# Optimization experiments

Hardware: AMD Instinct MI355X
Metric: run time of the kernel (lower is better)

Reference implementation:

```python
import jax, jax.numpy as jnp
import numpy as np

N_NODES = 100000
N_EDGES = 3200000
N_GRAPHS = 512


def setup_inputs() -> dict:
    key = jax.random.key(0)
    k1, k2, k3, k4, k5 = jax.random.split(key, 5)
    x = jax.random.normal(k1, (N_NODES, 5), dtype=jnp.float32)
    edge_index = jax.random.randint(k2, (2, N_EDGES), 0, N_NODES, dtype=jnp.int64)
    batch = jnp.sort(jax.random.randint(k3, (N_NODES,), 0, N_GRAPHS, dtype=jnp.int64))
    W1 = jax.random.normal(k4, (5, 16), dtype=jnp.float32) * (1.0 / np.sqrt(5.0))
    b1 = jnp.zeros((16,), dtype=jnp.float32)
    W2 = jax.random.normal(k5, (16, 16), dtype=jnp.float32) * 0.25
    b2 = jnp.zeros((16,), dtype=jnp.float32)
    return {"x": x, "edge_index": edge_index, "batch": batch,
            "W1": W1, "b1": b1, "W2": W2, "b2": b2}


def _gcn_conv(x, src, dst, norm, W, b, n_nodes):
    # PyG GCNConv: h = X W; out_i = sum_{j->i} norm_ij * h_j + b
    h = x @ W                                   # [N, out]
    msgs = h[src] * norm[:, None]               # gather + scale  [E_tot, out]
    out = jax.ops.segment_sum(msgs, dst, num_segments=n_nodes)
    return out + b


def reference(x, edge_index, batch, W1, b1, W2, b2):
    n = x.shape[0]
    # add self-loops (GCNConv default)
    loops = jnp.arange(n, dtype=edge_index.dtype)
    src = jnp.concatenate([edge_index[0], loops])
    dst = jnp.concatenate([edge_index[1], loops])
    # symmetric normalization: deg computed on destination nodes
    deg = jax.ops.segment_sum(jnp.ones_like(src, dtype=x.dtype), dst, num_segments=n)
    dinv = jnp.where(deg > 0, jax.lax.rsqrt(deg), 0.0)
    norm = dinv[src] * dinv[dst]                # [E_tot]

    h = jax.nn.relu(_gcn_conv(x, src, dst, norm, W1, b1, n))
    h = jax.nn.relu(_gcn_conv(h, src, dst, norm, W2, b2, n))

    # global mean pool over graphs in the batch
    sums = jax.ops.segment_sum(h, batch, num_segments=N_GRAPHS)
    cnts = jax.ops.segment_sum(jnp.ones((n,), dtype=h.dtype), batch, num_segments=N_GRAPHS)
    return sums / jnp.maximum(cnts, 1.0)[:, None]
```

## Files before the change

kernel.cpp:

```cpp
#include <hip/hip_runtime.h>

#define N_NODES  100000
#define N_EDGES  3200000
#define N_GRAPHS 512
#define F_IN     5
#define F_HID    16

#define PBLK   512
#define CHUNK  8192
#define NCHUNK ((N_EDGES + CHUNK - 1) / CHUNK)
#define BKT_NODES 256
#define NBKT ((N_NODES + BKT_NODES - 1) / BKT_NODES)
#define SHARDS 8
#define CAP_S  1280
#define CAP    (SHARDS * CAP_S)


__device__ inline unsigned short f2bf(float f) {
    unsigned u = __float_as_uint(f);
    return (unsigned short)((u + 0x7fffu + ((u >> 16) & 1u)) >> 16);
}
__device__ inline float bf2f(unsigned short h) {
    return __uint_as_float(((unsigned)h) << 16);
}
__device__ inline float4 cvt4(ushort4 u) {
    return make_float4(bf2f(u.x), bf2f(u.y), bf2f(u.z), bf2f(u.w));
}
__device__ inline float4 shfl_xor4(float4 v, int m) {
    return make_float4(__shfl_xor(v.x, m, 64), __shfl_xor(v.y, m, 64),
                       __shfl_xor(v.z, m, 64), __shfl_xor(v.w, m, 64));
}

template <int NW>
__device__ inline int block_incl_scan(int v, int t, int* wsum) {
    int lane = t & 63, wave = t >> 6;
    int x = v;
#pragma unroll
    for (int o = 1; o < 64; o <<= 1) {
        int y = __shfl_up(x, o, 64);
        if (lane >= o) x += y;
    }
    if (lane == 63) wsum[wave] = x;
    __syncthreads();
    if (t < 64) {
        int w = (t < NW) ? wsum[t] : 0;
#pragma unroll
        for (int o = 1; o < NW; o <<= 1) {
            int y = __shfl_up(w, o, 64);
            if (t >= o) w += y;
        }
        if (t < NW) wsum[t] = w;
    }
    __syncthreads();
    return x + (wave ? wsum[wave - 1] : 0);
}

__device__ inline float4 row_gather8s(const ushort4* __restrict__ pb4, int i, int j,
                                      int half, int beg, int len,
                                      const int* __restrict__ col) {
    float4 acc = half ? make_float4(0.f, 0.f, 0.f, 0.f)
                      : cvt4(pb4[i * 4 + j]);
    for (int k = half * 8; k < len; k += 16) {
        int4 c0 = *(const int4*)(col + beg + k);
        int4 c1 = *(const int4*)(col + beg + k + 4);
        ushort4 a0 = pb4[c0.x * 4 + j], a1 = pb4[c0.y * 4 + j];
        ushort4 a2 = pb4[c0.z * 4 + j], a3 = pb4[c0.w * 4 + j];
        ushort4 a4 = pb4[c1.x * 4 + j], a5 = pb4[c1.y * 4 + j];
        ushort4 a6 = pb4[c1.z * 4 + j], a7 = pb4[c1.w * 4 + j];
        float4 f0 = cvt4(a0), f1 = cvt4(a1), f2 = cvt4(a2), f3 = cvt4(a3);
        float4 f4 = cvt4(a4), f5 = cvt4(a5), f6 = cvt4(a6), f7 = cvt4(a7);
        acc.x += ((f0.x + f1.x) + (f2.x + f3.x)) + ((f4.x + f5.x) + (f6.x + f7.x));
        acc.y += ((f0.y + f1.y) + (f2.y + f3.y)) + ((f4.y + f5.y) + (f6.y + f7.y));
        acc.z += ((f0.z + f1.z) + (f2.z + f3.z)) + ((f4.z + f5.z) + (f6.z + f7.z));
        acc.w += ((f0.w + f1.w) + (f2.w + f3.w)) + ((f4.w + f5.w) + (f6.w + f7.w));
    }
    return acc;
}


__global__ void k_zero(int* __restrict__ cursor, float* __restrict__ out,
                       float* __restrict__ cnt, unsigned short* __restrict__ pb_a,
                       unsigned short* __restrict__ pb_b) {
    int i = blockIdx.x * blockDim.x + threadIdx.x;
    if (i < NBKT * SHARDS) cursor[i] = 0;
    if (i < N_GRAPHS * F_HID) out[i] = 0.0f;
    if (i < N_GRAPHS) cnt[i] = 0.0f;
    if (i < F_HID) {
        pb_a[(size_t)N_NODES * F_HID + i] = 0;
        pb_b[(size_t)N_NODES * F_HID + i] = 0;
    }
}

__global__ __launch_bounds__(PBLK) void k_part(const int* __restrict__ src,
                                               const int* __restrict__ dst,
                                               const int* __restrict__ batch,
                                               int* __restrict__ cursor,
                                               unsigned* __restrict__ packed,
                                               float* __restrict__ cnt) {
    __shared__ int hist[PBLK];
    __shared__ int scn[PBLK];
    __shared__ int rnk[PBLK];
    __shared__ int gbase[PBLK];
    __shared__ int wsum[8];
    __shared__ int bcnt[8];
    __shared__ int g0s;
    int t = threadIdx.x;
    int blk = blockIdx.x;
    int s = blk & (SHARDS - 1);
    int chunk0 = blk * CHUNK;
    int n = min(CHUNK, N_EDGES - chunk0);
    hist[t] = 0;
    if (t < 8) bcnt[t] = 0;
    if (t == 0) {
        int nb = blk * BKT_NODES;
        g0s = batch[nb < N_NODES ? nb : N_NODES - 1];
    }
    __syncthreads();
    int ls[CHUNK / PBLK], ld[CHUNK / PBLK];
    for (int k = t, idx = 0; k < n; k += PBLK, idx++) {
        ls[idx] = src[chunk0 + k];
        ld[idx] = dst[chunk0 + k];
        atomicAdd(&hist[ld[idx] >> 8], 1);
    }
    if (t < BKT_NODES) {
        int i2 = blk * BKT_NODES + t;
        if (i2 < N_NODES) {
            int g = batch[i2];
            int l = g - g0s;
            if (l >= 0 && l < 8) atomicAdd(&bcnt[l], 1);
            else atomicAdd(&cnt[g], 1.0f);
        }
    }
    __syncthreads();
    int v = hist[t];
    int incl = block_incl_scan<8>(v, t, wsum);
    int excl = incl - v;
    scn[t] = excl;
    rnk[t] = excl;
    gbase[t] = (v > 0) ? atomicAdd(&cursor[t * SHARDS + s], v) : 0;
    if (t < 8 && bcnt[t] > 0) atomicAdd(&cnt[g0s + t], (float)bcnt[t]);
    __syncthreads();
    for (int k = t, idx = 0; k < n; k += PBLK, idx++) {
        int d = ld[idx], sr = ls[idx];
        int b = d >> 8;
        int r = atomicAdd(&rnk[b], 1);
        int g = gbase[b] + (r - scn[b]);
        if (g < CAP_S)
            packed[(size_t)b * CAP + s * CAP_S + g] =
                ((unsigned)sr << 8) | (unsigned)(d & 255);
    }
}

__global__ __launch_bounds__(512) void k_csr(const int* __restrict__ cursor,
                                             const unsigned* __restrict__ packed,
                                             const float* __restrict__ x,
                                             const float* __restrict__ W1,
                                             int2* __restrict__ rowbc,
                                             int* __restrict__ col,
                                             float* __restrict__ dinv,
                                             unsigned short* __restrict__ pb) {
    __shared__ int hist[BKT_NODES];
    __shared__ int rnk[BKT_NODES];
    __shared__ int wsum[8];
    __shared__ int ns[SHARDS];
    __shared__ float w1[F_IN * F_HID];
    int b = blockIdx.x, t = threadIdx.x;
    int base = b * CAP;
    if (t < BKT_NODES) hist[t] = 0;
    if (t < SHARDS) ns[t] = min(cursor[b * SHARDS + t], CAP_S);
    if (t >= 512 - F_IN * F_HID) w1[t - (512 - F_IN * F_HID)] = W1[t - (512 - F_IN * F_HID)];
    __syncthreads();
    const unsigned* pk = packed + (size_t)b * CAP;
#pragma unroll
    for (int s = 0; s < SHARDS; s++) {
        int m = ns[s];
        const unsigned* pks = pk + s * CAP_S;
        for (int k = t; k < m; k += 512)
            atomicAdd(&hist[pks[k] & 255], 1);
    }
    __syncthreads();
    int v = (t < BKT_NODES) ? hist[t] : 0;
    int len = (v + 7) & ~7;
    int incl = block_incl_scan<8>(len, t, wsum);
    int excl = incl - len;
    if (t < BKT_NODES) rnk[t] = excl;
    __syncthreads();
#pragma unroll
    for (int s = 0; s < SHARDS; s++) {
        int m = ns[s];
        const unsigned* pks = pk + s * CAP_S;
        for (int k = t; k < m; k += 512) {
            unsigned w = pks[k];
            int r = atomicAdd(&rnk[w & 255], 1);
            if (r < CAP) col[base + r] = (int)(w >> 8);
        }
    }
    if (t < BKT_NODES) {
        int node = b * BKT_NODES + t;
        if (node < N_NODES) {
            int mylen = min(len, ((CAP - min(excl, CAP)) & ~7));
            for (int q = v; q < mylen; q++) {
                int r = excl + q;
                if (r < CAP) col[base + r] = N_NODES;
            }
            rowbc[node] = make_int2(base + excl, mylen);
            float di = rsqrtf((float)(1 + v));
            dinv[node] = di;
            float xi[F_IN];
#pragma unroll
            for (int k = 0; k < F_IN; k++) xi[k] = x[node * F_IN + k];
            float hv[F_HID];
#pragma unroll
            for (int c = 0; c < F_HID; c++) {
                float h = 0.0f;
#pragma unroll
                for (int k = 0; k < F_IN; k++) h += xi[k] * w1[k * F_HID + c];
                hv[c] = h * di;
            }
            unsigned pkk[8];
#pragma unroll
            for (int q = 0; q < 8; q++)
                pkk[q] = (unsigned)f2bf(hv[2 * q]) | ((unsigned)f2bf(hv[2 * q + 1]) << 16);
            uint4* d4 = (uint4*)(pb + (size_t)node * F_HID);
            d4[0] = make_uint4(pkk[0], pkk[1], pkk[2], pkk[3]);
            d4[1] = make_uint4(pkk[4], pkk[5], pkk[6], pkk[7]);
        }
    }
}

__global__ __launch_bounds__(256) void k_pull_mid(const int2* __restrict__ rowbc,
                                                  const int* __restrict__ col,
                                                  const unsigned short* __restrict__ pb,
                                                  const float* __restrict__ dinv,
                                                  const float* __restrict__ W2,
                                                  const float* __restrict__ b1,
                                                  unsigned short* __restrict__ pb2) {
    __shared__ float w[F_HID * F_HID];
    __shared__ float bb[F_HID];
    int t = threadIdx.x;
    w[t] = W2[t];
    if (t < F_HID) bb[t] = b1[t];
    __syncthreads();
    int gid = blockIdx.x * 256 + t;
    int i = gid >> 3;
    int half = (gid >> 2) & 1;
    int j = gid & 3;
    int2 rc = rowbc[i];
    float4 acc = row_gather8s((const ushort4*)pb, i, j, half, rc.x, rc.y, col);
    acc.x += __shfl_xor(acc.x, 4, 64);
    acc.y += __shfl_xor(acc.y, 4, 64);
    acc.z += __shfl_xor(acc.z, 4, 64);
    acc.w += __shfl_xor(acc.w, 4, 64);
    float di = dinv[i];
    float4 mine;
    mine.x = fmaxf(di * acc.x + bb[4 * j + 0], 0.0f);
    mine.y = fmaxf(di * acc.y + bb[4 * j + 1], 0.0f);
    mine.z = fmaxf(di * acc.z + bb[4 * j + 2], 0.0f);
    mine.w = fmaxf(di * acc.w + bb[4 * j + 3], 0.0f);
    float4 o1 = shfl_xor4(mine, 1);
    float4 o2 = shfl_xor4(mine, 2);
    float4 o3 = shfl_xor4(mine, 3);
    float4 hq0 = (j == 0) ? mine : ((j == 1) ? o1 : ((j == 2) ? o2 : o3));
    float4 hq1 = (j == 1) ? mine : ((j == 0) ? o1 : ((j == 3) ? o2 : o3));
    float4 hq2 = (j == 2) ? mine : ((j == 3) ? o1 : ((j == 0) ? o2 : o3));
    float4 hq3 = (j == 3) ? mine : ((j == 2) ? o1 : ((j == 1) ? o2 : o3));
    float hc[F_HID] = {hq0.x, hq0.y, hq0.z, hq0.w, hq1.x, hq1.y, hq1.z, hq1.w,
                       hq2.x, hq2.y, hq2.z, hq2.w, hq3.x, hq3.y, hq3.z, hq3.w};
    float m0 = 0.0f, m1 = 0.0f, m2 = 0.0f, m3 = 0.0f;
#pragma unroll
    for (int c = 0; c < F_HID; c++) {
        float4 wv = *(const float4*)&w[c * F_HID + 4 * j];
        float hv = hc[c];
        m0 += hv * wv.x; m1 += hv * wv.y; m2 += hv * wv.z; m3 += hv * wv.w;
    }
    if (half == 0) {
        unsigned p0 = (unsigned)f2bf(m0 * di) | ((unsigned)f2bf(m1 * di) << 16);
        unsigned p1 = (unsigned)f2bf(m2 * di) | ((unsigned)f2bf(m3 * di) << 16);
        *(uint2*)(pb2 + (size_t)i * F_HID + 4 * j) = make_uint2(p0, p1);
    }
}

__global__ __launch_bounds__(256) void k_pull_pool(const int2* __restrict__ rowbc,
                                                   const int* __restrict__ col,
                                                   const unsigned short* __restrict__ pb,
                                                   const float* __restrict__ dinv,
                                                   const int* __restrict__ batch,
                                                   const float* __restrict__ b2,
                                                   const float* __restrict__ cnt,
                                                   float* __restrict__ out) {
    __shared__ float bb[F_HID];
    __shared__ float acc2[8][F_HID];
    __shared__ int gcnt[8];
    __shared__ int g0s;
    int t = threadIdx.x;
    if (t < F_HID) bb[t] = b2[t];
    if (t < 8) gcnt[t] = 0;
    if (t < 8 * F_HID) ((float*)acc2)[t] = 0.0f;
    int blk0node = blockIdx.x * 32;
    if (t == 0) g0s = batch[blk0node < N_NODES ? blk0node : N_NODES - 1];
    __syncthreads();
    int g0 = g0s;
    int gid = blockIdx.x * 256 + t;
    int i = gid >> 3;
    int half = (gid >> 2) & 1;
    int j = gid & 3;
    int2 rc = rowbc[i];
    float4 acc = row_gather8s((const ushort4*)pb, i, j, half, rc.x, rc.y, col);
    acc.x += __shfl_xor(acc.x, 4, 64);
    acc.y += __shfl_xor(acc.y, 4, 64);
    acc.z += __shfl_xor(acc.z, 4, 64);
    acc.w += __shfl_xor(acc.w, 4, 64);
    if (half == 0) {
        float di = dinv[i];
        float h0 = fmaxf(di * acc.x + bb[4 * j + 0], 0.0f);
        float h1 = fmaxf(di * acc.y + bb[4 * j + 1], 0.0f);
        float h2 = fmaxf(di * acc.z + bb[4 * j + 2], 0.0f);
        float h3 = fmaxf(di * acc.w + bb[4 * j + 3], 0.0f);
        int g = batch[i];
        int l = g - g0;
        if (l >= 0 && l < 8) {
            atomicAdd(&acc2[l][4 * j + 0], h0);
            atomicAdd(&acc2[l][4 * j + 1], h1);
            atomicAdd(&acc2[l][4 * j + 2], h2);
            atomicAdd(&acc2[l][4 * j + 3], h3);
            if (j == 0) atomicAdd(&gcnt[l], 1);
        } else {
            float inv = 1.0f / cnt[g];
            atomicAdd(&out[g * F_HID + 4 * j + 0], h0 * inv);
            atomicAdd(&out[g * F_HID + 4 * j + 1], h1 * inv);
            atomicAdd(&out[g * F_HID + 4 * j + 2], h2 * inv);
            atomicAdd(&out[g * F_HID + 4 * j + 3], h3 * inv);
        }
    }
    __syncthreads();
    if (t < 8 * F_HID) {
        int l = t >> 4, c = t & 15;
        if (gcnt[l] > 0) {
            float inv = 1.0f / cnt[g0 + l];
            atomicAdd(&out[(g0 + l) * F_HID + c], acc2[l][c] * inv);
        }
    }
}


extern "C" void kernel_launch(void* const* d_in, const int* in_sizes, int n_in,
                              void* d_out, int out_size, void* d_ws, size_t ws_size,
                              hipStream_t stream) {
    const float* x     = (const float*)d_in[0];
    const int*   ei    = (const int*)d_in[1];
    const int*   batch = (const int*)d_in[2];
    const float* W1    = (const float*)d_in[3];
    const float* b1    = (const float*)d_in[4];
    const float* W2    = (const float*)d_in[5];
    const float* b2    = (const float*)d_in[6];
    float* out = (float*)d_out;

    int*            cursor = (int*)d_ws;
    unsigned*       packed = (unsigned*)(cursor + 3200);
    int2*           rowbc  = (int2*)(packed + (size_t)NBKT * CAP);
    int*            col    = (int*)(rowbc + N_NODES);
    float*          dinv   = (float*)(col + (size_t)NBKT * CAP);
    unsigned short* pb_a   = (unsigned short*)(dinv + N_NODES);
    unsigned short* pb_b   = pb_a + (size_t)(N_NODES + 1) * F_HID;
    float*          cnt    = (float*)(pb_b + (size_t)(N_NODES + 1) * F_HID);

    const int* src = ei;
    const int* dst = ei + N_EDGES;

    const int nb_pull = (N_NODES * 8) / 256;

    k_zero<<<(N_GRAPHS * F_HID + 255) / 256, 256, 0, stream>>>(cursor, out, cnt,
                                                               pb_a, pb_b);
    k_part<<<NCHUNK, PBLK, 0, stream>>>(src, dst, batch, cursor, packed, cnt);
    k_csr<<<NBKT, 512, 0, stream>>>(cursor, packed, x, W1, rowbc, col, dinv, pb_a);
    k_pull_mid<<<nb_pull, 256, 0, stream>>>(rowbc, col, pb_a, dinv, W2, b1, pb_b);
    k_pull_pool<<<nb_pull, 256, 0, stream>>>(rowbc, col, pb_b, dinv, batch, b2,
                                             cnt, out);
}
```

Before: 189.8 us.

## Reuse histogram atomic ranks in partition and CSR kernels to skip second atomic pass

Each edge now keeps the return value of its first shared-memory histogram atomicAdd as its local rank. This removes the block scan and the second atomic rank pass in k_part, and the reread of packed data in k_csr. k_part's chunk size is halved so more blocks run, and the per-block graph-count range shrinks to 128 nodes to match. k_csr holds its packed words in registers across the scan, which costs more registers and may lower occupancy.

```diff
diff --git a/kernel.cpp b/kernel.cpp
--- a/kernel.cpp
+++ b/kernel.cpp
@@ -7,13 +7,16 @@
 #define F_HID    16
 
 #define PBLK   512
-#define CHUNK  8192
+#define CHUNK  4096
+#define EPT    (CHUNK / PBLK)
 #define NCHUNK ((N_EDGES + CHUNK - 1) / CHUNK)
+#define CNT_NODES 128
 #define BKT_NODES 256
 #define NBKT ((N_NODES + BKT_NODES - 1) / BKT_NODES)
 #define SHARDS 8
 #define CAP_S  1280
 #define CAP    (SHARDS * CAP_S)
+#define UNR    (CAP / 512)
 
 
 __device__ inline unsigned short f2bf(float f) {
@@ -98,10 +101,7 @@
                                                unsigned* __restrict__ packed,
                                                float* __restrict__ cnt) {
     __shared__ int hist[PBLK];
-    __shared__ int scn[PBLK];
-    __shared__ int rnk[PBLK];
     __shared__ int gbase[PBLK];
-    __shared__ int wsum[8];
     __shared__ int bcnt[8];
     __shared__ int g0s;
     int t = threadIdx.x;
@@ -112,18 +112,22 @@
     hist[t] = 0;
     if (t < 8) bcnt[t] = 0;
     if (t == 0) {
-        int nb = blk * BKT_NODES;
+        int nb = blk * CNT_NODES;
         g0s = batch[nb < N_NODES ? nb : N_NODES - 1];
     }
     __syncthreads();
-    int ls[CHUNK / PBLK], ld[CHUNK / PBLK];
-    for (int k = t, idx = 0; k < n; k += PBLK, idx++) {
-        ls[idx] = src[chunk0 + k];
-        ld[idx] = dst[chunk0 + k];
-        atomicAdd(&hist[ld[idx] >> 8], 1);
-    }
-    if (t < BKT_NODES) {
-        int i2 = blk * BKT_NODES + t;
+    int ls[EPT], ld[EPT], lr[EPT];
+#pragma unroll
+    for (int idx = 0; idx < EPT; idx++) {
+        int k = t + idx * PBLK;
+        if (k < n) {
+            ls[idx] = src[chunk0 + k];
+            ld[idx] = dst[chunk0 + k];
+            lr[idx] = atomicAdd(&hist[ld[idx] >> 8], 1);
+        }
+    }
+    if (t < CNT_NODES) {
+        int i2 = blk * CNT_NODES + t;
         if (i2 < N_NODES) {
             int g = batch[i2];
             int l = g - g0s;
@@ -133,21 +137,19 @@
     }
     __syncthreads();
     int v = hist[t];
-    int incl = block_incl_scan<8>(v, t, wsum);
-    int excl = incl - v;
-    scn[t] = excl;
-    rnk[t] = excl;
     gbase[t] = (v > 0) ? atomicAdd(&cursor[t * SHARDS + s], v) : 0;
     if (t < 8 && bcnt[t] > 0) atomicAdd(&cnt[g0s + t], (float)bcnt[t]);
     __syncthreads();
-    for (int k = t, idx = 0; k < n; k += PBLK, idx++) {
-        int d = ld[idx], sr = ls[idx];
-        int b = d >> 8;
-        int r = atomicAdd(&rnk[b], 1);
-        int g = gbase[b] + (r - scn[b]);
-        if (g < CAP_S)
-            packed[(size_t)b * CAP + s * CAP_S + g] =
-                ((unsigned)sr << 8) | (unsigned)(d & 255);
+#pragma unroll
+    for (int idx = 0; idx < EPT; idx++) {
+        int k = t + idx * PBLK;
+        if (k < n) {
+            int b = ld[idx] >> 8;
+            int g = gbase[b] + lr[idx];
+            if (g < CAP_S)
+                packed[(size_t)b * CAP + s * CAP_S + g] =
+                    ((unsigned)ls[idx] << 8) | (unsigned)(ld[idx] & 255);
+        }
     }
 }
 
@@ -160,7 +162,7 @@
                                              float* __restrict__ dinv,
                                              unsigned short* __restrict__ pb) {
     __shared__ int hist[BKT_NODES];
-    __shared__ int rnk[BKT_NODES];
+    __shared__ int excl_s[BKT_NODES];
     __shared__ int wsum[8];
     __shared__ int ns[SHARDS];
     __shared__ float w1[F_IN * F_HID];
@@ -168,30 +170,34 @@
     int base = b * CAP;
     if (t < BKT_NODES) hist[t] = 0;
     if (t < SHARDS) ns[t] = min(cursor[b * SHARDS + t], CAP_S);
-    if (t >= 512 - F_IN * F_HID) w1[t - (512 - F_IN * F_HID)] = W1[t - (512 - F_IN * F_HID)];
+    if (t < F_IN * F_HID) w1[t] = W1[t];
     __syncthreads();
     const unsigned* pk = packed + (size_t)b * CAP;
-#pragma unroll
-    for (int s = 0; s < SHARDS; s++) {
-        int m = ns[s];
-        const unsigned* pks = pk + s * CAP_S;
-        for (int k = t; k < m; k += 512)
-            atomicAdd(&hist[pks[k] & 255], 1);
+    unsigned pv[UNR];
+    int pr[UNR];
+    unsigned okm = 0;
+#pragma unroll
+    for (int idx = 0; idx < UNR; idx++) {
+        int k = t + idx * 512;
+        int sh = k / CAP_S;
+        if ((k - sh * CAP_S) < ns[sh]) {
+            okm |= (1u << idx);
+            pv[idx] = pk[k];
+            pr[idx] = atomicAdd(&hist[pv[idx] & 255], 1);
+        }
     }
     __syncthreads();
     int v = (t < BKT_NODES) ? hist[t] : 0;
     int len = (v + 7) & ~7;
     int incl = block_incl_scan<8>(len, t, wsum);
     int excl = incl - len;
-    if (t < BKT_NODES) rnk[t] = excl;
-    __syncthreads();
-#pragma unroll
-    for (int s = 0; s < SHARDS; s++) {
-        int m = ns[s];
-        const unsigned* pks = pk + s * CAP_S;
-        for (int k = t; k < m; k += 512) {
-            unsigned w = pks[k];
-            int r = atomicAdd(&rnk[w & 255], 1);
+    if (t < BKT_NODES) excl_s[t] = excl;
+    __syncthreads();
+#pragma unroll
+    for (int idx = 0; idx < UNR; idx++) {
+        if (okm & (1u << idx)) {
+            unsigned w = pv[idx];
+            int r = excl_s[w & 255] + pr[idx];
             if (r < CAP) col[base + r] = (int)(w >> 8);
         }
     }
```

After: 190.0 us. No clear change (+0.1%).
